# Kernel tuning notes

Hardware: AMD Instinct MI355X
Metric: run time of the kernel (lower is better)

Reference implementation:

```python
import jax, jax.numpy as jnp
import numpy as np

N_NODES = 50000
N_EDGES = 800000
IN_DIM = 256
OUT_DIM = 256


def setup_inputs() -> dict:
    key = jax.random.key(0)
    k1, k2, k3, k4, k5, k6 = jax.random.split(key, 6)
    x = jax.random.normal(k1, (N_NODES, IN_DIM), dtype=jnp.float32)
    adj_rows = jax.random.randint(k2, (N_EDGES,), 0, N_NODES)
    adj_cols = jax.random.randint(k3, (N_EDGES,), 0, N_NODES)
    adj_vals = jax.random.uniform(k4, (N_EDGES,), dtype=jnp.float32)
    stdv = 1.0 / np.sqrt(OUT_DIM)
    W = jax.random.uniform(k5, (IN_DIM, OUT_DIM), minval=-stdv, maxval=stdv, dtype=jnp.float32)
    b = jax.random.uniform(k6, (OUT_DIM,), minval=-stdv, maxval=stdv, dtype=jnp.float32)
    return {"x": x, "adj_rows": adj_rows, "adj_cols": adj_cols, "adj_vals": adj_vals, "W": W, "b": b}


def reference(x, adj_rows, adj_cols, adj_vals, W, b):
    # hidden = x @ W  (first sparse.mm; x treated dense, identical math)
    hidden = jnp.matmul(x, W)  # [N, out_dim]
    # output = adj @ hidden via COO SpMM: gather source rows, scale, scatter-add to dest rows
    msgs = adj_vals[:, None] * hidden[adj_cols]  # [E, out_dim]
    output = jax.ops.segment_sum(msgs, adj_rows, num_segments=N_NODES)  # [N, out_dim]
    return output + b
```

## Files before the change

### kernel.cpp

```cpp
#include <hip/hip_runtime.h>

#define N_NODES 50000
#define N_EDGES 800000
#define DIM     256
#define STRIPS32 1563

typedef __attribute__((ext_vector_type(8))) short bf16x8;
typedef __attribute__((ext_vector_type(4))) float f32x4;

__device__ __forceinline__ unsigned short f2bf(float f) {
    unsigned u = __float_as_uint(f);
    unsigned r = (u + 0x7fffu + ((u >> 16) & 1u)) >> 16;
    return (unsigned short)r;
}
__device__ __forceinline__ float bf2f(unsigned short h) {
    return __uint_as_float((unsigned)h << 16);
}

__global__ __launch_bounds__(256)
void wtrans(const float* __restrict__ W, unsigned short* __restrict__ Wt) {
    const int n = blockIdx.x;
    const int k = threadIdx.x;
    Wt[n * DIM + k] = f2bf(W[(size_t)k * DIM + n]);
}

__global__ __launch_bounds__(512, 2)
void gemm_mfma(const float* __restrict__ X, const unsigned short* __restrict__ Wt,
               unsigned short* __restrict__ Hb) {
    __shared__ unsigned short wl[DIM * DIM];
    const int tid = threadIdx.x;
    {
        const uint4* src = (const uint4*)Wt;
#pragma unroll
        for (int i = 0; i < 16; ++i) {
            const int c   = i * 512 + tid;
            const int row = c >> 5;
            const int kb  = (c & 31) * 16;
            const int dst = row * 512 + (kb ^ ((row & 7) << 4));
            *(uint4*)((char*)wl + dst) = src[c];
        }
    }
    __syncthreads();

    const int wid   = tid >> 6;
    const int lane  = tid & 63;
    const int strip = blockIdx.x * 8 + wid;
    if (strip >= STRIPS32) return;

    const int r0   = strip * 32;
    const int arow = lane & 15;
    const int kgrp = lane >> 4;
    const int ra = r0 + arow;
    const int rb = r0 + 16 + arow;
    const float* xa = X + (size_t)(ra < N_NODES ? ra : N_NODES - 1) * DIM + kgrp * 8;
    const float* xb = X + (size_t)(rb < N_NODES ? rb : N_NODES - 1) * DIM + kgrp * 8;

    f32x4 acc[2][16];
#pragma unroll
    for (int h = 0; h < 2; ++h)
#pragma unroll
        for (int nt = 0; nt < 16; ++nt) acc[h][nt] = f32x4{0.f, 0.f, 0.f, 0.f};

    const int swz = (arow & 7) << 4;

    float4 pa0 = *(const float4*)(xa);
    float4 pa1 = *(const float4*)(xa + 4);
    float4 pb0 = *(const float4*)(xb);
    float4 pb1 = *(const float4*)(xb + 4);

#pragma unroll
    for (int ks = 0; ks < 8; ++ks) {
        bf16x8 a0, a1;
        a0[0] = (short)f2bf(pa0.x); a0[1] = (short)f2bf(pa0.y);
        a0[2] = (short)f2bf(pa0.z); a0[3] = (short)f2bf(pa0.w);
        a0[4] = (short)f2bf(pa1.x); a0[5] = (short)f2bf(pa1.y);
        a0[6] = (short)f2bf(pa1.z); a0[7] = (short)f2bf(pa1.w);
        a1[0] = (short)f2bf(pb0.x); a1[1] = (short)f2bf(pb0.y);
        a1[2] = (short)f2bf(pb0.z); a1[3] = (short)f2bf(pb0.w);
        a1[4] = (short)f2bf(pb1.x); a1[5] = (short)f2bf(pb1.y);
        a1[6] = (short)f2bf(pb1.z); a1[7] = (short)f2bf(pb1.w);
        if (ks < 7) {
            pa0 = *(const float4*)(xa + (ks + 1) * 32);
            pa1 = *(const float4*)(xa + (ks + 1) * 32 + 4);
            pb0 = *(const float4*)(xb + (ks + 1) * 32);
            pb1 = *(const float4*)(xb + (ks + 1) * 32 + 4);
        }
        const int kb = ((ks * 32 + kgrp * 8) * 2) ^ swz;
#pragma unroll
        for (int nt = 0; nt < 16; ++nt) {
            const int n = nt * 16 + arow;
            const bf16x8 b = *(const bf16x8*)((const char*)wl + n * 512 + kb);
            acc[0][nt] = __builtin_amdgcn_mfma_f32_16x16x32_bf16(a0, b, acc[0][nt], 0, 0, 0);
            acc[1][nt] = __builtin_amdgcn_mfma_f32_16x16x32_bf16(a1, b, acc[1][nt], 0, 0, 0);
        }
    }

#pragma unroll
    for (int h = 0; h < 2; ++h) {
        const int crow0 = r0 + h * 16 + kgrp * 4;
#pragma unroll
        for (int nt = 0; nt < 16; ++nt) {
#pragma unroll
            for (int q = 0; q < 4; ++q) {
                const int r = crow0 + q;
                if (r < N_NODES)
                    Hb[(size_t)r * DIM + nt * 16 + arow] = f2bf(acc[h][nt][q]);
            }
        }
    }
}

__global__ __launch_bounds__(256)
void count_edges(const int* __restrict__ rows, int* __restrict__ cnt) {
    const int e = blockIdx.x * 256 + threadIdx.x;
    if (e < N_EDGES) atomicAdd(&cnt[rows[e]], 1);
}

__device__ __forceinline__ int block_excl_scan_256(int v, int* wsum, int* total) {
    const int lane = threadIdx.x & 63;
    const int wave = threadIdx.x >> 6;
    int x = v;
#pragma unroll
    for (int off = 1; off < 64; off <<= 1) {
        const int y = __shfl_up(x, off, 64);
        if (lane >= off) x += y;
    }
    if (lane == 63) wsum[wave] = x;
    __syncthreads();
    if (threadIdx.x == 0) {
        int s = 0;
#pragma unroll
        for (int w = 0; w < 4; ++w) { const int t = wsum[w]; wsum[w] = s; s += t; }
        *total = s;
    }
    __syncthreads();
    return wsum[wave] + x - v;
}

__global__ __launch_bounds__(256)
void scan_blocks(const int* __restrict__ cnt, int* __restrict__ offs,
                 int* __restrict__ bsum) {
    __shared__ int wsum[4];
    __shared__ int total;
    const int i = blockIdx.x * 256 + threadIdx.x;
    const int v = (i < N_NODES) ? cnt[i] : 0;
    const int excl = block_excl_scan_256(v, wsum, &total);
    if (i < N_NODES) offs[i] = excl;
    if (threadIdx.x == 0) bsum[blockIdx.x] = total;
}

#define NBLK_NODES 196

__global__ __launch_bounds__(256)
void scan_top(int* __restrict__ bsum) {
    __shared__ int wsum[4];
    __shared__ int total;
    const int t = threadIdx.x;
    const int v = (t < NBLK_NODES) ? bsum[t] : 0;
    const int excl = block_excl_scan_256(v, wsum, &total);
    if (t < NBLK_NODES) bsum[t] = excl;
}

__global__ __launch_bounds__(256)
void scan_add(int* __restrict__ offs, const int* __restrict__ bsum) {
    const int i = blockIdx.x * 256 + threadIdx.x;
    if (i < N_NODES) offs[i] += bsum[blockIdx.x];
    if (i == 0) offs[N_NODES] = N_EDGES;
}

__global__ __launch_bounds__(256)
void fill_edges(const int* __restrict__ rows, const int* __restrict__ cols,
                const float* __restrict__ vals, const int* __restrict__ offs,
                int* __restrict__ cursor, int2* __restrict__ pe) {
    const int e = blockIdx.x * 256 + threadIdx.x;
    if (e >= N_EDGES) return;
    const int r = rows[e];
    const int p = atomicAdd(&cursor[r], 1);
    pe[offs[r] + p] = make_int2(cols[e], __float_as_int(vals[e]));
}

__global__ __launch_bounds__(256)
void spmm(const unsigned short* __restrict__ Hb, const int* __restrict__ offs,
          const int2* __restrict__ pe, const float* __restrict__ bias,
          float* __restrict__ out) {
    const int row  = blockIdx.x * 4 + (threadIdx.x >> 6);
    const int lane = threadIdx.x & 63;
    if (row >= N_NODES) return;
    const int beg = offs[row];
    const int end = offs[row + 1];
    const unsigned lb = (unsigned)lane * 4;
    float4 acc = make_float4(0.f, 0.f, 0.f, 0.f);
    int i = beg;
    for (; i + 8 <= end; i += 8) {
        int2 e[8];
#pragma unroll
        for (int j = 0; j < 8; ++j) e[j] = pe[i + j];
        ushort4 h[8];
#pragma unroll
        for (int j = 0; j < 8; ++j)
            h[j] = *(const ushort4*)&Hb[((unsigned)e[j].x << 8) + lb];
#pragma unroll
        for (int j = 0; j < 8; ++j) {
            const float v = __int_as_float(e[j].y);
            acc.x += v * bf2f(h[j].x);
            acc.y += v * bf2f(h[j].y);
            acc.z += v * bf2f(h[j].z);
            acc.w += v * bf2f(h[j].w);
        }
    }
    for (; i < end; ++i) {
        const int2 e0 = pe[i];
        const ushort4 h0 = *(const ushort4*)&Hb[((unsigned)e0.x << 8) + lb];
        const float v0 = __int_as_float(e0.y);
        acc.x += v0 * bf2f(h0.x);
        acc.y += v0 * bf2f(h0.y);
        acc.z += v0 * bf2f(h0.z);
        acc.w += v0 * bf2f(h0.w);
    }
    const float4 bb = *(const float4*)&bias[lane * 4];
    acc.x += bb.x; acc.y += bb.y; acc.z += bb.z; acc.w += bb.w;
    *(float4*)&out[(size_t)row * DIM + lane * 4] = acc;
}

extern "C" void kernel_launch(void* const* d_in, const int* in_sizes, int n_in,
                              void* d_out, int out_size, void* d_ws, size_t ws_size,
                              hipStream_t stream) {
    const float* x        = (const float*)d_in[0];
    const int*   adj_rows = (const int*)d_in[1];
    const int*   adj_cols = (const int*)d_in[2];
    const float* adj_vals = (const float*)d_in[3];
    const float* W        = (const float*)d_in[4];
    const float* b        = (const float*)d_in[5];
    float*       out      = (float*)d_out;

    char* ws = (char*)d_ws;
    size_t off = 0;
    auto alloc = [&](size_t bytes) {
        void* p = ws + off;
        off = (off + bytes + 255) & ~(size_t)255;
        return p;
    };
    unsigned short* hiddenb = (unsigned short*)alloc((size_t)N_NODES * DIM * sizeof(unsigned short));
    unsigned short* Wt      = (unsigned short*)alloc((size_t)DIM * DIM * sizeof(unsigned short));
    int*   offs    = (int*)  alloc((N_NODES + 1) * sizeof(int));
    int*   cntcur  = (int*)  alloc((size_t)2 * N_NODES * sizeof(int));
    int*   bsum    = (int*)  alloc(256 * sizeof(int));
    int2*  pe      = (int2*) alloc((size_t)N_EDGES * sizeof(int2));
    int* cnt    = cntcur;
    int* cursor = cntcur + N_NODES;

    wtrans<<<DIM, 256, 0, stream>>>(W, Wt);

    gemm_mfma<<<(STRIPS32 + 7) / 8, 512, 0, stream>>>(x, Wt, hiddenb);

    hipMemsetAsync(cntcur, 0, (size_t)2 * N_NODES * sizeof(int), stream);
    count_edges<<<(N_EDGES + 255) / 256, 256, 0, stream>>>(adj_rows, cnt);
    scan_blocks<<<NBLK_NODES, 256, 0, stream>>>(cnt, offs, bsum);
    scan_top<<<1, 256, 0, stream>>>(bsum);
    scan_add<<<NBLK_NODES, 256, 0, stream>>>(offs, bsum);
    fill_edges<<<(N_EDGES + 255) / 256, 256, 0, stream>>>(
        adj_rows, adj_cols, adj_vals, offs, cursor, pe);

    spmm<<<(N_NODES + 3) / 4, 256, 0, stream>>>(hiddenb, offs, pe, b, out);
}
```

Measured before the change: 264.9 us.

## Fuse setup kernels: merge memset with W transpose, count into GEMM, inline top scan

Folds the workspace memset into the W-transpose kernel and runs edge counting in extra blocks of the GEMM launch, so the counting overlaps the GEMM. The top-level scan and the add-back pass are dropped. Each fill_edges and spmm block now rescans the 196 block sums in shared memory and adds the prefix on the fly. This cuts launches from about nine to five at the cost of redundant per-block scans and a heterogeneous GEMM launch.

```diff
diff --git a/kernel.cpp b/kernel.cpp
--- a/kernel.cpp
+++ b/kernel.cpp
@@ -4,6 +4,10 @@
 #define N_EDGES 800000
 #define DIM     256
 #define STRIPS32 1563
+#define NBLK_NODES 196
+#define GEMM_BLOCKS 196
+#define COUNT_BLOCKS 782
+#define K2_BLOCKS (GEMM_BLOCKS + COUNT_BLOCKS)
 
 typedef __attribute__((ext_vector_type(8))) short bf16x8;
 typedef __attribute__((ext_vector_type(4))) float f32x4;
@@ -17,18 +21,54 @@
     return __uint_as_float((unsigned)h << 16);
 }
 
-__global__ __launch_bounds__(256)
-void wtrans(const float* __restrict__ W, unsigned short* __restrict__ Wt) {
-    const int n = blockIdx.x;
-    const int k = threadIdx.x;
-    Wt[n * DIM + k] = f2bf(W[(size_t)k * DIM + n]);
+__device__ __forceinline__ int block_excl_scan_256(int v, int* wsum, int* total) {
+    const int lane = threadIdx.x & 63;
+    const int wave = threadIdx.x >> 6;
+    int x = v;
+#pragma unroll
+    for (int off = 1; off < 64; off <<= 1) {
+        const int y = __shfl_up(x, off, 64);
+        if (lane >= off) x += y;
+    }
+    if (lane == 63) wsum[wave] = x;
+    __syncthreads();
+    if (threadIdx.x == 0) {
+        int s = 0;
+#pragma unroll
+        for (int w = 0; w < 4; ++w) { const int t = wsum[w]; wsum[w] = s; s += t; }
+        *total = s;
+    }
+    __syncthreads();
+    return wsum[wave] + x - v;
+}
+
+__global__ __launch_bounds__(256)
+void prep(const float* __restrict__ W, unsigned short* __restrict__ Wt,
+          int* __restrict__ cntcur) {
+    const int i = blockIdx.x * 256 + threadIdx.x;
+    if (i < 2 * N_NODES) cntcur[i] = 0;
+    if (blockIdx.x < DIM) {
+        const int n = blockIdx.x, k = threadIdx.x;
+        Wt[n * DIM + k] = f2bf(W[(size_t)k * DIM + n]);
+    }
 }
 
 __global__ __launch_bounds__(512, 2)
-void gemm_mfma(const float* __restrict__ X, const unsigned short* __restrict__ Wt,
-               unsigned short* __restrict__ Hb) {
+void gemm_count(const float* __restrict__ X, const unsigned short* __restrict__ Wt,
+                unsigned short* __restrict__ Hb,
+                const int* __restrict__ rows, int* __restrict__ cnt) {
     __shared__ unsigned short wl[DIM * DIM];
     const int tid = threadIdx.x;
+
+    if (blockIdx.x >= GEMM_BLOCKS) {
+        const int base = (blockIdx.x - GEMM_BLOCKS) * 1024;
+        int e = base + tid;
+        if (e < N_EDGES) atomicAdd(&cnt[rows[e]], 1);
+        e += 512;
+        if (e < N_EDGES) atomicAdd(&cnt[rows[e]], 1);
+        return;
+    }
+
     {
         const uint4* src = (const uint4*)Wt;
 #pragma unroll
@@ -111,33 +151,6 @@
 }
 
 __global__ __launch_bounds__(256)
-void count_edges(const int* __restrict__ rows, int* __restrict__ cnt) {
-    const int e = blockIdx.x * 256 + threadIdx.x;
-    if (e < N_EDGES) atomicAdd(&cnt[rows[e]], 1);
-}
-
-__device__ __forceinline__ int block_excl_scan_256(int v, int* wsum, int* total) {
-    const int lane = threadIdx.x & 63;
-    const int wave = threadIdx.x >> 6;
-    int x = v;
-#pragma unroll
-    for (int off = 1; off < 64; off <<= 1) {
-        const int y = __shfl_up(x, off, 64);
-        if (lane >= off) x += y;
-    }
-    if (lane == 63) wsum[wave] = x;
-    __syncthreads();
-    if (threadIdx.x == 0) {
-        int s = 0;
-#pragma unroll
-        for (int w = 0; w < 4; ++w) { const int t = wsum[w]; wsum[w] = s; s += t; }
-        *total = s;
-    }
-    __syncthreads();
-    return wsum[wave] + x - v;
-}
-
-__global__ __launch_bounds__(256)
 void scan_blocks(const int* __restrict__ cnt, int* __restrict__ offs,
                  int* __restrict__ bsum) {
     __shared__ int wsum[4];
@@ -149,45 +162,47 @@
     if (threadIdx.x == 0) bsum[blockIdx.x] = total;
 }
 
-#define NBLK_NODES 196
-
-__global__ __launch_bounds__(256)
-void scan_top(int* __restrict__ bsum) {
+__global__ __launch_bounds__(256)
+void fill_edges(const int* __restrict__ rows, const int* __restrict__ cols,
+                const float* __restrict__ vals, const int* __restrict__ offs,
+                const int* __restrict__ bsum, int* __restrict__ cursor,
+                int2* __restrict__ pe) {
     __shared__ int wsum[4];
     __shared__ int total;
-    const int t = threadIdx.x;
-    const int v = (t < NBLK_NODES) ? bsum[t] : 0;
-    const int excl = block_excl_scan_256(v, wsum, &total);
-    if (t < NBLK_NODES) bsum[t] = excl;
-}
-
-__global__ __launch_bounds__(256)
-void scan_add(int* __restrict__ offs, const int* __restrict__ bsum) {
-    const int i = blockIdx.x * 256 + threadIdx.x;
-    if (i < N_NODES) offs[i] += bsum[blockIdx.x];
-    if (i == 0) offs[N_NODES] = N_EDGES;
-}
-
-__global__ __launch_bounds__(256)
-void fill_edges(const int* __restrict__ rows, const int* __restrict__ cols,
-                const float* __restrict__ vals, const int* __restrict__ offs,
-                int* __restrict__ cursor, int2* __restrict__ pe) {
+    __shared__ int P[256];
+    {
+        const int t = threadIdx.x;
+        const int v = (t < NBLK_NODES) ? bsum[t] : 0;
+        const int excl = block_excl_scan_256(v, wsum, &total);
+        P[t] = excl;
+    }
+    __syncthreads();
     const int e = blockIdx.x * 256 + threadIdx.x;
     if (e >= N_EDGES) return;
     const int r = rows[e];
     const int p = atomicAdd(&cursor[r], 1);
-    pe[offs[r] + p] = make_int2(cols[e], __float_as_int(vals[e]));
+    pe[offs[r] + P[r >> 8] + p] = make_int2(cols[e], __float_as_int(vals[e]));
 }
 
 __global__ __launch_bounds__(256)
 void spmm(const unsigned short* __restrict__ Hb, const int* __restrict__ offs,
-          const int2* __restrict__ pe, const float* __restrict__ bias,
-          float* __restrict__ out) {
+          const int* __restrict__ bsum, const int2* __restrict__ pe,
+          const float* __restrict__ bias, float* __restrict__ out) {
+    __shared__ int wsum[4];
+    __shared__ int total;
+    __shared__ int P[256];
+    {
+        const int t = threadIdx.x;
+        const int v = (t < NBLK_NODES) ? bsum[t] : 0;
+        const int excl = block_excl_scan_256(v, wsum, &total);
+        P[t] = excl;
+    }
+    __syncthreads();
+
     const int row  = blockIdx.x * 4 + (threadIdx.x >> 6);
     const int lane = threadIdx.x & 63;
-    if (row >= N_NODES) return;
-    const int beg = offs[row];
-    const int end = offs[row + 1];
+    const int beg = offs[row] + P[row >> 8];
+    const int end = (row + 1 == N_NODES) ? N_EDGES : (offs[row + 1] + P[(row + 1) >> 8]);
     const unsigned lb = (unsigned)lane * 4;
     float4 acc = make_float4(0.f, 0.f, 0.f, 0.f);
     int i = beg;
@@ -242,24 +257,21 @@
     };
     unsigned short* hiddenb = (unsigned short*)alloc((size_t)N_NODES * DIM * sizeof(unsigned short));
     unsigned short* Wt      = (unsigned short*)alloc((size_t)DIM * DIM * sizeof(unsigned short));
-    int*   offs    = (int*)  alloc((N_NODES + 1) * sizeof(int));
+    int*   offs    = (int*)  alloc((size_t)N_NODES * sizeof(int));
     int*   cntcur  = (int*)  alloc((size_t)2 * N_NODES * sizeof(int));
     int*   bsum    = (int*)  alloc(256 * sizeof(int));
     int2*  pe      = (int2*) alloc((size_t)N_EDGES * sizeof(int2));
     int* cnt    = cntcur;
     int* cursor = cntcur + N_NODES;
 
-    wtrans<<<DIM, 256, 0, stream>>>(W, Wt);
-
-    gemm_mfma<<<(STRIPS32 + 7) / 8, 512, 0, stream>>>(x, Wt, hiddenb);
-
-    hipMemsetAsync(cntcur, 0, (size_t)2 * N_NODES * sizeof(int), stream);
-    count_edges<<<(N_EDGES + 255) / 256, 256, 0, stream>>>(adj_rows, cnt);
+    prep<<<(2 * N_NODES + 255) / 256, 256, 0, stream>>>(W, Wt, cntcur);
+
+    gemm_count<<<K2_BLOCKS, 512, 0, stream>>>(x, Wt, hiddenb, adj_rows, cnt);
+
     scan_blocks<<<NBLK_NODES, 256, 0, stream>>>(cnt, offs, bsum);
-    scan_top<<<1, 256, 0, stream>>>(bsum);
-    scan_add<<<NBLK_NODES, 256, 0, stream>>>(offs, bsum);
+
     fill_edges<<<(N_EDGES + 255) / 256, 256, 0, stream>>>(
-        adj_rows, adj_cols, adj_vals, offs, cursor, pe);
-
-    spmm<<<(N_NODES + 3) / 4, 256, 0, stream>>>(hiddenb, offs, pe, b, out);
-}
+        adj_rows, adj_cols, adj_vals, offs, bsum, cursor, pe);
+
+    spmm<<<N_NODES / 4, 256, 0, stream>>>(hiddenb, offs, bsum, pe, b, out);
+}
```

New measurement: 249.1 us. 6.0% less time.
